# Performance work log

Measured on AMD Instinct MI355X. Metric: run time of the kernel, lower is better.

## Reference

```python
import jax, jax.numpy as jnp
import numpy as np

K, d = 8, 8
D = K * d          # 64
B, T, N = 8, 12, 325


def _xavier(key, shape):
    fan_out, fan_in = shape
    lim = (6.0 / (fan_in + fan_out)) ** 0.5
    return jax.random.uniform(key, shape, jnp.float32, -lim, lim)


def setup_inputs() -> dict:
    key = jax.random.key(0)
    ks = jax.random.split(key, 8)
    return {
        "X": jax.random.normal(ks[0], (B, T, N, D), jnp.float32),
        "STE": jax.random.normal(ks[1], (B, T, N, D), jnp.float32),
        "adj": jax.random.randint(ks[2], (N, N), 0, 2, jnp.int32),
        "W7": _xavier(ks[3], (D, 2 * D)), "b7": jnp.zeros((D,), jnp.float32),
        "W8": _xavier(ks[4], (D, 2 * D)), "b8": jnp.zeros((D,), jnp.float32),
        "W9": _xavier(ks[5], (D, 2 * D)), "b9": jnp.zeros((D,), jnp.float32),
        "W10": _xavier(ks[6], (D, D)), "b10": jnp.zeros((D,), jnp.float32),
        "W11": _xavier(ks[7], (D, D)), "b11": jnp.zeros((D,), jnp.float32),
    }


def reference(X, STE, adj, W7, b7, W8, b8, W9, b9, W10, b10, W11, b11):
    # X, STE: [B, T, N, D]
    x = jnp.concatenate([X, STE], axis=-1)  # [B,T,N,2D]
    gelu = lambda t: jax.nn.gelu(t, approximate=False)  # torch F.gelu default = exact erf
    q = gelu(x @ W7.T + b7)  # [B,T,N,D]
    k = gelu(x @ W8.T + b8)
    v = gelu(x @ W9.T + b9)
    # split D into K heads of size d (equivalent to torch split(dim=-1)+cat(dim=0))
    heads = lambda t: t.reshape(B, T, N, K, d)
    q, k, v = heads(q), heads(k), heads(v)
    # scores: [K,B,T,N,N] == torch's [K*B,T,N,N]
    attn = jnp.einsum('btnkd,btmkd->kbtnm', q, k) / (d ** 0.5)
    attn = jnp.where(adj > 0, attn, jnp.float32(-9e15))
    attn = jax.nn.softmax(attn, axis=-1)
    out = jnp.einsum('kbtnm,btmkd->btnkd', attn, v).reshape(B, T, N, D)
    out = gelu(out @ W10.T + b10) @ W11.T + b11
    return out
```

## Files before the change

### kernel.cpp

```cpp
#include <hip/hip_runtime.h>
#include <math.h>

#define NN 325
#define BT 96
#define NROWS (BT * NN)
#define SCL (0.35355339059327373f * 1.4426950408889634f)

typedef _Float16 half_t;
typedef half_t half4_t __attribute__((ext_vector_type(4)));
typedef half_t half2_t __attribute__((ext_vector_type(2)));
typedef float float4_t __attribute__((ext_vector_type(4)));

__device__ __forceinline__ float gelu_f(float x) {
    return 0.5f * x * (1.0f + erff(x * 0.70710678118654752f));
}

__global__ void prep_kernel(const int* __restrict__ adj,
                            const float* __restrict__ W7,
                            const float* __restrict__ W8,
                            const float* __restrict__ W9,
                            const float* __restrict__ W10,
                            const float* __restrict__ W11,
                            unsigned int* __restrict__ packedT,
                            half_t* __restrict__ w789,
                            half_t* __restrict__ wab)
{
    int idx = blockIdx.x * 256 + threadIdx.x;
    if (idx < 11 * NN) {
        int w = idx / NN, n = idx - w * NN;
        unsigned int bits = 0u;
        #pragma unroll 8
        for (int j = 0; j < 32; ++j) {
            int m = w * 32 + j;
            if (m < NN && adj[n * NN + m] > 0) bits |= (1u << j);
        }
        packedT[w * NN + n] = bits;
    } else if (idx < 3575 + 24576) {
        int i = idx - 3575;
        int p = i >> 13, r = i & 8191;
        const float* Wp = (p == 0) ? W7 : (p == 1) ? W8 : W9;
        w789[i] = (half_t)Wp[r];
    } else if (idx < 3575 + 24576 + 8192) {
        int i = idx - 28151;
        int p = i >> 12, r = i & 4095;
        wab[i] = (half_t)(p ? W11[r] : W10[r]);
    }
}

#define XS 136

__device__ __forceinline__ void qkv_stage_w(const half_t* __restrict__ src,
                                            half_t* dst, int tid)
{
    #pragma unroll
    for (int idx = tid; idx < 1024; idx += 512) {
        int c = idx >> 4, g = idx & 15;
        *(uint4*)&dst[c * XS + g * 8] = *(const uint4*)&src[c * 128 + g * 8];
    }
}

__device__ __forceinline__ void qkv_compute(
    const half_t* x16, const half_t* wb, const float* __restrict__ b,
    half_t* __restrict__ outp, float oscale,
    int row0, int rbase, int ch, int l15, int quad)
{
    float4_t acc[2];
    #pragma unroll
    for (int cc = 0; cc < 2; ++cc) {
        float bias = b[(ch * 2 + cc) * 16 + l15];
        acc[cc] = (float4_t){bias, bias, bias, bias};
    }
    #pragma unroll
    for (int kk = 0; kk < 8; ++kk) {
        half4_t a = *(const half4_t*)&x16[(rbase + l15) * XS + kk * 16 + quad * 4];
        #pragma unroll
        for (int cc = 0; cc < 2; ++cc) {
            half4_t bf = *(const half4_t*)
                &wb[((ch * 2 + cc) * 16 + l15) * XS + kk * 16 + quad * 4];
            acc[cc] = __builtin_amdgcn_mfma_f32_16x16x16f16(a, bf, acc[cc], 0, 0, 0);
        }
    }
    #pragma unroll
    for (int cc = 0; cc < 2; ++cc) {
        #pragma unroll
        for (int rr = 0; rr < 4; ++rr) {
            int R = row0 + rbase + quad * 4 + rr;
            if (R < NROWS)
                outp[R * 64 + (ch * 2 + cc) * 16 + l15] =
                    (half_t)(gelu_f(acc[cc][rr]) * oscale);
        }
    }
}

__global__ __launch_bounds__(512) void qkv_kernel(
    const float* __restrict__ X, const float* __restrict__ STE,
    const half_t* __restrict__ w789,
    const float* __restrict__ b7, const float* __restrict__ b8,
    const float* __restrict__ b9,
    half_t* __restrict__ q, half_t* __restrict__ k, half_t* __restrict__ v)
{
    __shared__ __attribute__((aligned(16))) half_t x16[64 * XS];
    __shared__ __attribute__((aligned(16))) half_t wbuf[2][64 * XS];
    const int tid  = threadIdx.x;
    const int row0 = blockIdx.x * 64;

    #pragma unroll
    for (int idx = tid; idx < 2048; idx += 512) {
        int r = idx >> 5, c4 = idx & 31;
        int R = row0 + r;
        float4 f = {0.f, 0.f, 0.f, 0.f};
        if (R < NROWS)
            f = (c4 < 16) ? *(const float4*)(X + R * 64 + c4 * 4)
                          : *(const float4*)(STE + R * 64 + (c4 - 16) * 4);
        half4_t hv;
        hv[0] = (half_t)f.x; hv[1] = (half_t)f.y;
        hv[2] = (half_t)f.z; hv[3] = (half_t)f.w;
        *(half4_t*)&x16[r * XS + c4 * 4] = hv;
    }
    qkv_stage_w(w789, wbuf[0], tid);
    __syncthreads();

    const int lane = tid & 63, wv = tid >> 6;
    const int l15 = lane & 15, quad = lane >> 4;
    const int rbase = (wv & 3) * 16, ch = wv >> 2;

    qkv_stage_w(w789 + 8192, wbuf[1], tid);
    qkv_compute(x16, wbuf[0], b7, q, SCL, row0, rbase, ch, l15, quad);
    __syncthreads();

    qkv_stage_w(w789 + 16384, wbuf[0], tid);
    qkv_compute(x16, wbuf[1], b8, k, 1.0f, row0, rbase, ch, l15, quad);
    __syncthreads();

    qkv_compute(x16, wbuf[0], b9, v, 1.0f, row0, rbase, ch, l15, quad);
}

__global__ __launch_bounds__(256) void attn_kernel(
    const half_t* __restrict__ q16g, const half_t* __restrict__ k16g,
    const half_t* __restrict__ v16g, const unsigned int* __restrict__ packedT,
    half_t* __restrict__ ao)
{
    __shared__ __attribute__((aligned(16))) half_t K16[336 * 20];
    __shared__ __attribute__((aligned(16))) half_t VT16[16 * 344];
    const int tid = threadIdx.x;
    const int h = blockIdx.x, bt = blockIdx.y;
    const long base = (long)(bt * NN) * 64 + h * 8;

    const half4_t z4 = {(half_t)0.f, (half_t)0.f, (half_t)0.f, (half_t)0.f};

    for (int idx = tid; idx < 16 * 344 / 2; idx += 256)
        ((half2_t*)VT16)[idx] = (half2_t)(half_t)0.f;
    __syncthreads();
    for (int i = tid; i < 344; i += 256)
        VT16[8 * 344 + i] = (half_t)1.0f;

    for (int r = tid; r < 336; r += 256) {
        half4_t ka = z4, kb = z4;
        if (r < NN) {
            ka = *(const half4_t*)(k16g + base + r * 64);
            kb = *(const half4_t*)(k16g + base + r * 64 + 4);
        }
        *(half4_t*)&K16[r * 20]      = ka;
        *(half4_t*)&K16[r * 20 + 4]  = kb;
        *(half4_t*)&K16[r * 20 + 8]  = z4;
        *(half4_t*)&K16[r * 20 + 12] = z4;
    }

    for (int mp = tid; mp < 168; mp += 256) {
        int m0 = 2 * mp, m1 = 2 * mp + 1;
        half4_t v0a = z4, v0b = z4, v1a = z4, v1b = z4;
        if (m0 < NN) {
            v0a = *(const half4_t*)(v16g + base + m0 * 64);
            v0b = *(const half4_t*)(v16g + base + m0 * 64 + 4);
        }
        if (m1 < NN) {
            v1a = *(const half4_t*)(v16g + base + m1 * 64);
            v1b = *(const half4_t*)(v16g + base + m1 * 64 + 4);
        }
        #pragma unroll
        for (int c = 0; c < 4; ++c) {
            half2_t p0; p0[0] = v0a[c]; p0[1] = v1a[c];
            half2_t p1; p1[0] = v0b[c]; p1[1] = v1b[c];
            *(half2_t*)&VT16[c * 344 + 2 * mp]       = p0;
            *(half2_t*)&VT16[(c + 4) * 344 + 2 * mp] = p1;
        }
    }
    __syncthreads();

    const int lane = tid & 63;
    const int wv   = tid >> 6;
    const int l15  = lane & 15;
    const int quad = lane >> 4;
    const int qsh  = quad * 4;

    for (int t = wv; t < 21; t += 4) {
        const int n  = t * 16 + l15;
        const int nq = (n < NN) ? n : (NN - 1);

        half4_t qf = z4;
        if (quad < 2)
            qf = *(const half4_t*)(q16g + base + (long)nq * 64 + qsh);

        float rm = 0.0f;
        #pragma unroll
        for (int mt = 0; mt < 21; ++mt) {
            half4_t kf = *(const half4_t*)&K16[(mt * 16 + l15) * 20 + qsh];
            float4_t s = __builtin_amdgcn_mfma_f32_16x16x16f16(
                kf, qf, (float4_t){0.f, 0.f, 0.f, 0.f}, 0, 0, 0);
            rm = fmaxf(rm, fmaxf(fmaxf(s[0], s[1]), fmaxf(s[2], s[3])));
        }
        rm = fmaxf(rm, __shfl_xor(rm, 16, 64));
        rm = fmaxf(rm, __shfl_xor(rm, 32, 64));

        unsigned int mb[11];
        #pragma unroll
        for (int w = 0; w < 11; ++w) mb[w] = packedT[w * NN + nq];

        const float4_t cinit = {-rm, -rm, -rm, -rm};
        float4_t acc = {0.f, 0.f, 0.f, 0.f};
        #pragma unroll
        for (int mt = 0; mt < 21; ++mt) {
            half4_t kf = *(const half4_t*)&K16[(mt * 16 + l15) * 20 + qsh];
            float4_t s = __builtin_amdgcn_mfma_f32_16x16x16f16(
                kf, qf, cinit, 0, 0, 0);
            unsigned int sh = mb[mt >> 1] >> (((mt & 1) << 4) + qsh);
            float p0 = (sh & 1u) ? __builtin_amdgcn_exp2f(s[0]) : 0.f;
            float p1 = (sh & 2u) ? __builtin_amdgcn_exp2f(s[1]) : 0.f;
            float p2 = (sh & 4u) ? __builtin_amdgcn_exp2f(s[2]) : 0.f;
            float p3 = (sh & 8u) ? __builtin_amdgcn_exp2f(s[3]) : 0.f;
            half4_t pf;
            pf[0] = (half_t)p0; pf[1] = (half_t)p1;
            pf[2] = (half_t)p2; pf[3] = (half_t)p3;
            half4_t vf = *(const half4_t*)&VT16[l15 * 344 + mt * 16 + qsh];
            acc = __builtin_amdgcn_mfma_f32_16x16x16f16(vf, pf, acc, 0, 0, 0);
        }

        float sum = __shfl(acc[0], 32 + l15, 64);

        if (quad < 2 && n < NN) {
            float inv = 1.0f / sum;
            half4_t o;
            o[0] = (half_t)(acc[0] * inv); o[1] = (half_t)(acc[1] * inv);
            o[2] = (half_t)(acc[2] * inv); o[3] = (half_t)(acc[3] * inv);
            *(half4_t*)(ao + base + (long)n * 64 + qsh) = o;
        }
    }
}

#define PS 72

__global__ __launch_bounds__(512) void proj_kernel(
    const half_t* __restrict__ ao, const half_t* __restrict__ wab,
    const float* __restrict__ b10, const float* __restrict__ b11,
    float* __restrict__ out)
{
    __shared__ __attribute__((aligned(16))) half_t a16[64 * PS];
    __shared__ __attribute__((aligned(16))) half_t wA[64 * PS];
    __shared__ __attribute__((aligned(16))) half_t wB[64 * PS];
    __shared__ __attribute__((aligned(16))) half_t h16[64 * PS];
    const int tid  = threadIdx.x;
    const int row0 = blockIdx.x * 64;

    for (int idx = tid; idx < 512; idx += 512) {
        int r = idx >> 3, c8 = idx & 7;
        int R = row0 + r;
        uint4 u = {0u, 0u, 0u, 0u};
        if (R < NROWS) u = *(const uint4*)(ao + (long)R * 64 + c8 * 8);
        *(uint4*)&a16[r * PS + c8 * 8] = u;
        *(uint4*)&wA[r * PS + c8 * 8] = *(const uint4*)&wab[r * 64 + c8 * 8];
        *(uint4*)&wB[r * PS + c8 * 8] = *(const uint4*)&wab[4096 + r * 64 + c8 * 8];
    }
    __syncthreads();

    const int lane = tid & 63, wv = tid >> 6;
    const int l15 = lane & 15, quad = lane >> 4;
    const int rbase = (wv & 3) * 16, ch = wv >> 2;

    float4_t acc[2];
    #pragma unroll
    for (int cc = 0; cc < 2; ++cc) {
        float bias = b10[(ch * 2 + cc) * 16 + l15];
        acc[cc] = (float4_t){bias, bias, bias, bias};
    }
    #pragma unroll
    for (int kk = 0; kk < 4; ++kk) {
        half4_t a = *(const half4_t*)&a16[(rbase + l15) * PS + kk * 16 + quad * 4];
        #pragma unroll
        for (int cc = 0; cc < 2; ++cc) {
            half4_t bf = *(const half4_t*)
                &wA[((ch * 2 + cc) * 16 + l15) * PS + kk * 16 + quad * 4];
            acc[cc] = __builtin_amdgcn_mfma_f32_16x16x16f16(a, bf, acc[cc], 0, 0, 0);
        }
    }
    #pragma unroll
    for (int cc = 0; cc < 2; ++cc) {
        #pragma unroll
        for (int rr = 0; rr < 4; ++rr)
            h16[(rbase + quad * 4 + rr) * PS + (ch * 2 + cc) * 16 + l15] =
                (half_t)gelu_f(acc[cc][rr]);
    }
    __syncthreads();

    #pragma unroll
    for (int cc = 0; cc < 2; ++cc) {
        float bias = b11[(ch * 2 + cc) * 16 + l15];
        acc[cc] = (float4_t){bias, bias, bias, bias};
    }
    #pragma unroll
    for (int kk = 0; kk < 4; ++kk) {
        half4_t a = *(const half4_t*)&h16[(rbase + l15) * PS + kk * 16 + quad * 4];
        #pragma unroll
        for (int cc = 0; cc < 2; ++cc) {
            half4_t bf = *(const half4_t*)
                &wB[((ch * 2 + cc) * 16 + l15) * PS + kk * 16 + quad * 4];
            acc[cc] = __builtin_amdgcn_mfma_f32_16x16x16f16(a, bf, acc[cc], 0, 0, 0);
        }
    }
    #pragma unroll
    for (int cc = 0; cc < 2; ++cc) {
        #pragma unroll
        for (int rr = 0; rr < 4; ++rr) {
            int R = row0 + rbase + quad * 4 + rr;
            if (R < NROWS)
                out[R * 64 + (ch * 2 + cc) * 16 + l15] = acc[cc][rr];
        }
    }
}

extern "C" void kernel_launch(void* const* d_in, const int* in_sizes, int n_in,
                              void* d_out, int out_size, void* d_ws, size_t ws_size,
                              hipStream_t stream) {
    const float* X   = (const float*)d_in[0];
    const float* STE = (const float*)d_in[1];
    const int*   adj = (const int*)d_in[2];
    const float* W7  = (const float*)d_in[3];
    const float* b7  = (const float*)d_in[4];
    const float* W8  = (const float*)d_in[5];
    const float* b8  = (const float*)d_in[6];
    const float* W9  = (const float*)d_in[7];
    const float* b9  = (const float*)d_in[8];
    const float* W10 = (const float*)d_in[9];
    const float* b10 = (const float*)d_in[10];
    const float* W11 = (const float*)d_in[11];
    const float* b11 = (const float*)d_in[12];

    char* wsb = (char*)d_ws;
    const long S = (long)NROWS * 64;
    half_t* qb = (half_t*)wsb;
    half_t* kb = qb + S;
    half_t* vb = qb + 2 * S;
    half_t* ab = qb + 3 * S;
    unsigned int* pk = (unsigned int*)(wsb + 4 * S * sizeof(half_t));
    half_t* w789 = (half_t*)(wsb + 4 * S * sizeof(half_t) + 16384);
    half_t* wab  = w789 + 24576;

    prep_kernel<<<142, 256, 0, stream>>>(adj, W7, W8, W9, W10, W11,
                                         pk, w789, wab);
    qkv_kernel<<<dim3((NROWS + 63) / 64), 512, 0, stream>>>(
        X, STE, w789, b7, b8, b9, qb, kb, vb);
    attn_kernel<<<dim3(8, BT), 256, 0, stream>>>(qb, kb, vb, pk, ab);
    proj_kernel<<<dim3((NROWS + 63) / 64), 512, 0, stream>>>(
        ab, wab, b10, b11, (float*)d_out);
}
```

Baseline: 153.2 us.

## Split attention query tiles across grid z and halve qkv/proj row tiles

The attention grid gains a third dimension of 3, so each block handles 7 of the 21 query tiles and the block count triples. The qkv and proj kernels move from 64-row, 512-thread blocks to 32-row, 256-thread blocks (975 blocks), and qkv drops its weight double buffer in favour of a single buffer with extra barriers. Row-bound checks are removed because 31200 rows divide evenly by 32. The aim is more blocks to fill the CUs, at the cost of each attention block re-staging the full K/V into shared memory and qkv losing its overlap of weight staging with compute.

Measured after the change: 162.6 us. 1.06x slower.

```diff
diff --git a/kernel.cpp b/kernel.cpp
--- a/kernel.cpp
+++ b/kernel.cpp
@@ -53,7 +53,7 @@
                                             half_t* dst, int tid)
 {
     #pragma unroll
-    for (int idx = tid; idx < 1024; idx += 512) {
+    for (int idx = tid; idx < 1024; idx += 256) {
         int c = idx >> 4, g = idx & 15;
         *(uint4*)&dst[c * XS + g * 8] = *(const uint4*)&src[c * 128 + g * 8];
     }
@@ -85,54 +85,51 @@
         #pragma unroll
         for (int rr = 0; rr < 4; ++rr) {
             int R = row0 + rbase + quad * 4 + rr;
-            if (R < NROWS)
-                outp[R * 64 + (ch * 2 + cc) * 16 + l15] =
-                    (half_t)(gelu_f(acc[cc][rr]) * oscale);
-        }
-    }
-}
-
-__global__ __launch_bounds__(512) void qkv_kernel(
+            outp[R * 64 + (ch * 2 + cc) * 16 + l15] =
+                (half_t)(gelu_f(acc[cc][rr]) * oscale);
+        }
+    }
+}
+
+__global__ __launch_bounds__(256) void qkv_kernel(
     const float* __restrict__ X, const float* __restrict__ STE,
     const half_t* __restrict__ w789,
     const float* __restrict__ b7, const float* __restrict__ b8,
     const float* __restrict__ b9,
     half_t* __restrict__ q, half_t* __restrict__ k, half_t* __restrict__ v)
 {
-    __shared__ __attribute__((aligned(16))) half_t x16[64 * XS];
-    __shared__ __attribute__((aligned(16))) half_t wbuf[2][64 * XS];
+    __shared__ __attribute__((aligned(16))) half_t x16[32 * XS];
+    __shared__ __attribute__((aligned(16))) half_t wbuf[64 * XS];
     const int tid  = threadIdx.x;
-    const int row0 = blockIdx.x * 64;
-
-    #pragma unroll
-    for (int idx = tid; idx < 2048; idx += 512) {
+    const int row0 = blockIdx.x * 32;
+
+    #pragma unroll
+    for (int idx = tid; idx < 1024; idx += 256) {
         int r = idx >> 5, c4 = idx & 31;
         int R = row0 + r;
-        float4 f = {0.f, 0.f, 0.f, 0.f};
-        if (R < NROWS)
-            f = (c4 < 16) ? *(const float4*)(X + R * 64 + c4 * 4)
-                          : *(const float4*)(STE + R * 64 + (c4 - 16) * 4);
+        float4 f = (c4 < 16) ? *(const float4*)(X + (long)R * 64 + c4 * 4)
+                             : *(const float4*)(STE + (long)R * 64 + (c4 - 16) * 4);
         half4_t hv;
         hv[0] = (half_t)f.x; hv[1] = (half_t)f.y;
         hv[2] = (half_t)f.z; hv[3] = (half_t)f.w;
         *(half4_t*)&x16[r * XS + c4 * 4] = hv;
     }
-    qkv_stage_w(w789, wbuf[0], tid);
+    qkv_stage_w(w789, wbuf, tid);
     __syncthreads();
 
     const int lane = tid & 63, wv = tid >> 6;
     const int l15 = lane & 15, quad = lane >> 4;
-    const int rbase = (wv & 3) * 16, ch = wv >> 2;
-
-    qkv_stage_w(w789 + 8192, wbuf[1], tid);
-    qkv_compute(x16, wbuf[0], b7, q, SCL, row0, rbase, ch, l15, quad);
-    __syncthreads();
-
-    qkv_stage_w(w789 + 16384, wbuf[0], tid);
-    qkv_compute(x16, wbuf[1], b8, k, 1.0f, row0, rbase, ch, l15, quad);
-    __syncthreads();
-
-    qkv_compute(x16, wbuf[0], b9, v, 1.0f, row0, rbase, ch, l15, quad);
+    const int rbase = (wv & 1) * 16, ch = wv >> 1;
+
+    qkv_compute(x16, wbuf, b7, q, SCL, row0, rbase, ch, l15, quad);
+    __syncthreads();
+    qkv_stage_w(w789 + 8192, wbuf, tid);
+    __syncthreads();
+    qkv_compute(x16, wbuf, b8, k, 1.0f, row0, rbase, ch, l15, quad);
+    __syncthreads();
+    qkv_stage_w(w789 + 16384, wbuf, tid);
+    __syncthreads();
+    qkv_compute(x16, wbuf, b9, v, 1.0f, row0, rbase, ch, l15, quad);
 }
 
 __global__ __launch_bounds__(256) void attn_kernel(
@@ -143,7 +140,7 @@
     __shared__ __attribute__((aligned(16))) half_t K16[336 * 20];
     __shared__ __attribute__((aligned(16))) half_t VT16[16 * 344];
     const int tid = threadIdx.x;
-    const int h = blockIdx.x, bt = blockIdx.y;
+    const int h = blockIdx.x, bt = blockIdx.y, z = blockIdx.z;
     const long base = (long)(bt * NN) * 64 + h * 8;
 
     const half4_t z4 = {(half_t)0.f, (half_t)0.f, (half_t)0.f, (half_t)0.f};
@@ -193,7 +190,7 @@
     const int quad = lane >> 4;
     const int qsh  = quad * 4;
 
-    for (int t = wv; t < 21; t += 4) {
+    for (int t = z * 7 + wv; t < z * 7 + 7; t += 4) {
         const int n  = t * 16 + l15;
         const int nq = (n < NN) ? n : (NN - 1);
 
@@ -249,24 +246,27 @@
 
 #define PS 72
 
-__global__ __launch_bounds__(512) void proj_kernel(
+__global__ __launch_bounds__(256) void proj_kernel(
     const half_t* __restrict__ ao, const half_t* __restrict__ wab,
     const float* __restrict__ b10, const float* __restrict__ b11,
     float* __restrict__ out)
 {
-    __shared__ __attribute__((aligned(16))) half_t a16[64 * PS];
+    __shared__ __attribute__((aligned(16))) half_t a16[32 * PS];
+    __shared__ __attribute__((aligned(16))) half_t h16[32 * PS];
     __shared__ __attribute__((aligned(16))) half_t wA[64 * PS];
     __shared__ __attribute__((aligned(16))) half_t wB[64 * PS];
-    __shared__ __attribute__((aligned(16))) half_t h16[64 * PS];
     const int tid  = threadIdx.x;
-    const int row0 = blockIdx.x * 64;
-
-    for (int idx = tid; idx < 512; idx += 512) {
+    const int row0 = blockIdx.x * 32;
+
+    #pragma unroll
+    for (int idx = tid; idx < 256; idx += 256) {
         int r = idx >> 3, c8 = idx & 7;
-        int R = row0 + r;
-        uint4 u = {0u, 0u, 0u, 0u};
-        if (R < NROWS) u = *(const uint4*)(ao + (long)R * 64 + c8 * 8);
-        *(uint4*)&a16[r * PS + c8 * 8] = u;
+        *(uint4*)&a16[r * PS + c8 * 8] =
+            *(const uint4*)(ao + (long)(row0 + r) * 64 + c8 * 8);
+    }
+    #pragma unroll
+    for (int idx = tid; idx < 512; idx += 256) {
+        int r = idx >> 3, c8 = idx & 7;
         *(uint4*)&wA[r * PS + c8 * 8] = *(const uint4*)&wab[r * 64 + c8 * 8];
         *(uint4*)&wB[r * PS + c8 * 8] = *(const uint4*)&wab[4096 + r * 64 + c8 * 8];
     }
@@ -274,7 +274,7 @@
 
     const int lane = tid & 63, wv = tid >> 6;
     const int l15 = lane & 15, quad = lane >> 4;
-    const int rbase = (wv & 3) * 16, ch = wv >> 2;
+    const int rbase = (wv & 1) * 16, ch = wv >> 1;
 
     float4_t acc[2];
     #pragma unroll
@@ -321,8 +321,7 @@
         #pragma unroll
         for (int rr = 0; rr < 4; ++rr) {
             int R = row0 + rbase + quad * 4 + rr;
-            if (R < NROWS)
-                out[R * 64 + (ch * 2 + cc) * 16 + l15] = acc[cc][rr];
+            out[R * 64 + (ch * 2 + cc) * 16 + l15] = acc[cc][rr];
         }
     }
 }
@@ -356,9 +355,9 @@
 
     prep_kernel<<<142, 256, 0, stream>>>(adj, W7, W8, W9, W10, W11,
                                          pk, w789, wab);
-    qkv_kernel<<<dim3((NROWS + 63) / 64), 512, 0, stream>>>(
+    qkv_kernel<<<dim3(975), 256, 0, stream>>>(
         X, STE, w789, b7, b8, b9, qb, kb, vb);
-    attn_kernel<<<dim3(8, BT), 256, 0, stream>>>(qb, kb, vb, pk, ab);
-    proj_kernel<<<dim3((NROWS + 63) / 64), 512, 0, stream>>>(
+    attn_kernel<<<dim3(8, BT, 3), 256, 0, stream>>>(qb, kb, vb, pk, ab);
+    proj_kernel<<<dim3(975), 256, 0, stream>>>(
         ab, wab, b10, b11, (float*)d_out);
 }
```

## Fold prep kernel into qkv kernel and pad V transpose stride

Applied to the files above, without the earlier changes.

Removes the separate prep launch. Each qkv block now converts W7/W8/W9 from fp32 to fp16 while staging them into shared memory, and one extra block (index 488) packs the adjacency bitmask and converts W10/W11 for later kernels. This saves a kernel launch and the round trip through the fp16 weight buffer, but every block now repeats the weight conversion, and the extra block's serial adjacency packing may lengthen the tail. The VT16 shared stride also changes from 344 to 348, which looks aimed at reducing LDS bank conflicts.

After: 234.2 us. 1.53x slower.

```diff
diff --git a/kernel.cpp b/kernel.cpp
--- a/kernel.cpp
+++ b/kernel.cpp
@@ -15,47 +15,19 @@
     return 0.5f * x * (1.0f + erff(x * 0.70710678118654752f));
 }
 
-__global__ void prep_kernel(const int* __restrict__ adj,
-                            const float* __restrict__ W7,
-                            const float* __restrict__ W8,
-                            const float* __restrict__ W9,
-                            const float* __restrict__ W10,
-                            const float* __restrict__ W11,
-                            unsigned int* __restrict__ packedT,
-                            half_t* __restrict__ w789,
-                            half_t* __restrict__ wab)
-{
-    int idx = blockIdx.x * 256 + threadIdx.x;
-    if (idx < 11 * NN) {
-        int w = idx / NN, n = idx - w * NN;
-        unsigned int bits = 0u;
-        #pragma unroll 8
-        for (int j = 0; j < 32; ++j) {
-            int m = w * 32 + j;
-            if (m < NN && adj[n * NN + m] > 0) bits |= (1u << j);
-        }
-        packedT[w * NN + n] = bits;
-    } else if (idx < 3575 + 24576) {
-        int i = idx - 3575;
-        int p = i >> 13, r = i & 8191;
-        const float* Wp = (p == 0) ? W7 : (p == 1) ? W8 : W9;
-        w789[i] = (half_t)Wp[r];
-    } else if (idx < 3575 + 24576 + 8192) {
-        int i = idx - 28151;
-        int p = i >> 12, r = i & 4095;
-        wab[i] = (half_t)(p ? W11[r] : W10[r]);
-    }
-}
-
 #define XS 136
 
-__device__ __forceinline__ void qkv_stage_w(const half_t* __restrict__ src,
-                                            half_t* dst, int tid)
-{
-    #pragma unroll
-    for (int idx = tid; idx < 1024; idx += 512) {
-        int c = idx >> 4, g = idx & 15;
-        *(uint4*)&dst[c * XS + g * 8] = *(const uint4*)&src[c * 128 + g * 8];
+__device__ __forceinline__ void qkv_stage_w32(const float* __restrict__ src,
+                                              half_t* dst, int tid)
+{
+    #pragma unroll
+    for (int idx = tid; idx < 2048; idx += 512) {
+        int c = idx >> 5, g = idx & 31;
+        float4 f = *(const float4*)&src[c * 128 + g * 4];
+        half4_t hv;
+        hv[0] = (half_t)f.x; hv[1] = (half_t)f.y;
+        hv[2] = (half_t)f.z; hv[3] = (half_t)f.w;
+        *(half4_t*)&dst[c * XS + g * 4] = hv;
     }
 }
 
@@ -94,14 +66,35 @@
 
 __global__ __launch_bounds__(512) void qkv_kernel(
     const float* __restrict__ X, const float* __restrict__ STE,
-    const half_t* __restrict__ w789,
+    const float* __restrict__ W7, const float* __restrict__ W8,
+    const float* __restrict__ W9,
     const float* __restrict__ b7, const float* __restrict__ b8,
     const float* __restrict__ b9,
-    half_t* __restrict__ q, half_t* __restrict__ k, half_t* __restrict__ v)
-{
+    const int* __restrict__ adj,
+    const float* __restrict__ W10, const float* __restrict__ W11,
+    half_t* __restrict__ q, half_t* __restrict__ k, half_t* __restrict__ v,
+    unsigned int* __restrict__ packedT, half_t* __restrict__ wab)
+{
+    const int tid = threadIdx.x;
+
+    if (blockIdx.x == 488) {
+        for (int idx = tid; idx < 11 * NN; idx += 512) {
+            int w = idx / NN, n = idx - w * NN;
+            unsigned int bits = 0u;
+            #pragma unroll 8
+            for (int j = 0; j < 32; ++j) {
+                int m = w * 32 + j;
+                if (m < NN && adj[n * NN + m] > 0) bits |= (1u << j);
+            }
+            packedT[w * NN + n] = bits;
+        }
+        for (int idx = tid; idx < 8192; idx += 512)
+            wab[idx] = (half_t)((idx < 4096) ? W10[idx] : W11[idx - 4096]);
+        return;
+    }
+
     __shared__ __attribute__((aligned(16))) half_t x16[64 * XS];
     __shared__ __attribute__((aligned(16))) half_t wbuf[2][64 * XS];
-    const int tid  = threadIdx.x;
     const int row0 = blockIdx.x * 64;
 
     #pragma unroll
@@ -117,23 +110,25 @@
         hv[2] = (half_t)f.z; hv[3] = (half_t)f.w;
         *(half4_t*)&x16[r * XS + c4 * 4] = hv;
     }
-    qkv_stage_w(w789, wbuf[0], tid);
+    qkv_stage_w32(W7, wbuf[0], tid);
     __syncthreads();
 
     const int lane = tid & 63, wv = tid >> 6;
     const int l15 = lane & 15, quad = lane >> 4;
     const int rbase = (wv & 3) * 16, ch = wv >> 2;
 
-    qkv_stage_w(w789 + 8192, wbuf[1], tid);
+    qkv_stage_w32(W8, wbuf[1], tid);
     qkv_compute(x16, wbuf[0], b7, q, SCL, row0, rbase, ch, l15, quad);
     __syncthreads();
 
-    qkv_stage_w(w789 + 16384, wbuf[0], tid);
+    qkv_stage_w32(W9, wbuf[0], tid);
     qkv_compute(x16, wbuf[1], b8, k, 1.0f, row0, rbase, ch, l15, quad);
     __syncthreads();
 
     qkv_compute(x16, wbuf[0], b9, v, 1.0f, row0, rbase, ch, l15, quad);
 }
+
+#define VS 348
 
 __global__ __launch_bounds__(256) void attn_kernel(
     const half_t* __restrict__ q16g, const half_t* __restrict__ k16g,
@@ -141,18 +136,18 @@
     half_t* __restrict__ ao)
 {
     __shared__ __attribute__((aligned(16))) half_t K16[336 * 20];
-    __shared__ __attribute__((aligned(16))) half_t VT16[16 * 344];
+    __shared__ __attribute__((aligned(16))) half_t VT16[16 * VS];
     const int tid = threadIdx.x;
     const int h = blockIdx.x, bt = blockIdx.y;
     const long base = (long)(bt * NN) * 64 + h * 8;
 
     const half4_t z4 = {(half_t)0.f, (half_t)0.f, (half_t)0.f, (half_t)0.f};
 
-    for (int idx = tid; idx < 16 * 344 / 2; idx += 256)
+    for (int idx = tid; idx < 16 * VS / 2; idx += 256)
         ((half2_t*)VT16)[idx] = (half2_t)(half_t)0.f;
     __syncthreads();
-    for (int i = tid; i < 344; i += 256)
-        VT16[8 * 344 + i] = (half_t)1.0f;
+    for (int i = tid; i < VS; i += 256)
+        VT16[8 * VS + i] = (half_t)1.0f;
 
     for (int r = tid; r < 336; r += 256) {
         half4_t ka = z4, kb = z4;
@@ -181,8 +176,8 @@
         for (int c = 0; c < 4; ++c) {
             half2_t p0; p0[0] = v0a[c]; p0[1] = v1a[c];
             half2_t p1; p1[0] = v0b[c]; p1[1] = v1b[c];
-            *(half2_t*)&VT16[c * 344 + 2 * mp]       = p0;
-            *(half2_t*)&VT16[(c + 4) * 344 + 2 * mp] = p1;
+            *(half2_t*)&VT16[c * VS + 2 * mp]       = p0;
+            *(half2_t*)&VT16[(c + 4) * VS + 2 * mp] = p1;
         }
     }
     __syncthreads();
@@ -231,7 +226,7 @@
             half4_t pf;
             pf[0] = (half_t)p0; pf[1] = (half_t)p1;
             pf[2] = (half_t)p2; pf[3] = (half_t)p3;
-            half4_t vf = *(const half4_t*)&VT16[l15 * 344 + mt * 16 + qsh];
+            half4_t vf = *(const half4_t*)&VT16[l15 * VS + mt * 16 + qsh];
             acc = __builtin_amdgcn_mfma_f32_16x16x16f16(vf, pf, acc, 0, 0, 0);
         }
 
@@ -351,13 +346,11 @@
     half_t* vb = qb + 2 * S;
     half_t* ab = qb + 3 * S;
     unsigned int* pk = (unsigned int*)(wsb + 4 * S * sizeof(half_t));
-    half_t* w789 = (half_t*)(wsb + 4 * S * sizeof(half_t) + 16384);
-    half_t* wab  = w789 + 24576;
-
-    prep_kernel<<<142, 256, 0, stream>>>(adj, W7, W8, W9, W10, W11,
-                                         pk, w789, wab);
-    qkv_kernel<<<dim3((NROWS + 63) / 64), 512, 0, stream>>>(
-        X, STE, w789, b7, b8, b9, qb, kb, vb);
+    half_t* wab = (half_t*)(wsb + 4 * S * sizeof(half_t) + 16384);
+
+    qkv_kernel<<<dim3(489), 512, 0, stream>>>(
+        X, STE, W7, W8, W9, b7, b8, b9, adj, W10, W11,
+        qb, kb, vb, pk, wab);
     attn_kernel<<<dim3(8, BT), 256, 0, stream>>>(qb, kb, vb, pk, ab);
     proj_kernel<<<dim3((NROWS + 63) / 64), 512, 0, stream>>>(
         ab, wab, b10, b11, (float*)d_out);
```
